# Optimization experiments

Measured on AMD Instinct MI355X. Metric: run time of the kernel, lower is better.

The kernel has to match this reference:

```python
import jax, jax.numpy as jnp
import numpy as np

KS = 7
DIM = 1024
HEADS = 16
B = 2048

def _rpb_index(ks):
    # Replicates the torch buffer: relative_position_index, shape [ks*ks, ks*ks]
    ch = np.arange(ks)
    coords = np.stack(np.meshgrid(ch, ch, indexing='ij')).reshape(2, -1)  # [2, N]
    rel = coords[:, :, None] - coords[:, None, :]                          # [2, N, N]
    rel = rel.transpose(1, 2, 0).copy()                                    # [N, N, 2]
    rel[:, :, 0] += ks - 1
    rel[:, :, 1] += ks - 1
    rel[:, :, 0] *= 2 * ks - 1
    idx = np.flipud(np.fliplr(rel.sum(-1)))
    return jnp.asarray(idx.copy())

def setup_inputs() -> dict:
    key = jax.random.key(0)
    ks = jax.random.split(key, 4)
    x = jax.random.normal(ks[0], (B, KS, KS, DIM), dtype=jnp.float32)
    qkv_w = jax.random.normal(ks[1], (3 * DIM, DIM), dtype=jnp.float32) * (DIM ** -0.5)
    qkv_b = jnp.zeros((3 * DIM,), dtype=jnp.float32)
    rpb = jax.random.normal(ks[2], (HEADS, 2 * KS - 1, 2 * KS - 1), dtype=jnp.float32) * 0.02
    proj_w = jax.random.normal(ks[3], (DIM, DIM), dtype=jnp.float32) * (DIM ** -0.5)
    proj_b = jnp.zeros((DIM,), dtype=jnp.float32)
    return {"x": x, "qkv_w": qkv_w, "qkv_b": qkv_b, "rpb": rpb, "proj_w": proj_w, "proj_b": proj_b}

def reference(x, qkv_w, qkv_b, rpb, proj_w, proj_b):
    Bn, H, W, C = x.shape
    ksz = H
    N = H * W
    heads = rpb.shape[0]
    hd = C // heads
    scale = hd ** -0.5
    idx = _rpb_index(ksz)  # [N, N] int

    qkv = x.reshape(Bn, N, C) @ qkv_w.T + qkv_b              # [B, N, 3C]
    qkv = qkv.reshape(Bn, N, 3, heads, hd).transpose(2, 0, 3, 1, 4)  # [3, B, h, N, hd]
    q, k, v = qkv[0] * scale, qkv[1], qkv[2]

    attn = jnp.einsum('bhnd,bhmd->bhnm', q, k)               # [B, h, N, N]
    # gather relative-position bias: rpb[h, 2k-1, 2k-1] -> flat [(2k-1)^2, h] -> [N, N, h]
    bias = rpb.transpose(1, 2, 0).reshape(-1, heads)[idx.reshape(-1)]
    bias = bias.reshape(N, N, heads).transpose(2, 0, 1)      # [h, N, N]
    attn = jax.nn.softmax(attn + bias[None], axis=-1)

    out = jnp.einsum('bhnm,bhmd->bhnd', attn, v)             # [B, h, N, hd]
    out = out.transpose(0, 2, 1, 3).reshape(Bn, H, W, C)
    return out @ proj_w.T + proj_b
```

## Files before the change

### kernel.cpp

```cpp
#include <hip/hip_runtime.h>


typedef _Float16 f16;
typedef _Float16 f16x8 __attribute__((ext_vector_type(8)));
typedef _Float16 f16x4 __attribute__((ext_vector_type(4)));
typedef float f32x4 __attribute__((ext_vector_type(4)));

#define G1P(p) ((const __attribute__((address_space(1))) unsigned int*)(p))
#define L3P(p) ((__attribute__((address_space(3))) unsigned int*)(p))

static const size_t MROW_MAX = 100351;

__global__ void cvt_kernel(const float* __restrict__ in, f16* __restrict__ out, int n4) {
  int i = blockIdx.x * blockDim.x + threadIdx.x;
  int stride = gridDim.x * blockDim.x;
  const float4* in4 = (const float4*)in;
  f16x4* out4 = (f16x4*)out;
  for (; i < n4; i += stride) {
    float4 v = in4[i];
    f16x4 o = { (f16)v.x, (f16)v.y, (f16)v.z, (f16)v.w };
    out4[i] = o;
  }
}

__global__ void bias_kernel(const float* __restrict__ rpb, float* __restrict__ bias_all) {
  int h = blockIdx.x;
  for (int e = threadIdx.x; e < 4096; e += blockDim.x) {
    int n = e >> 6, m = e & 63;
    float v = -1e30f;
    if (n < 49 && m < 49) {
      int in_ = n / 7, jn = n % 7, im = m / 7, jm = m % 7;
      v = rpb[h * 169 + (im - in_ + 6) * 13 + (jm - jn + 6)];
    }
    bias_all[h * 4096 + e] = v;
  }
}


#define VM4 asm volatile("s_waitcnt vmcnt(4)" ::: "memory")
#define VM0 asm volatile("s_waitcnt vmcnt(0)" ::: "memory")
#define NOVM ((void)0)
#define NOSTG ((void)0)

#define STAGE(GB, ROW0, COL0, LDSOFF)                                              \
  {                                                                                \
    const f16* s0_ = (GB) + (size_t)((ROW0) + wid * 32 + srow) * K + ((COL0) + sce); \
    __builtin_amdgcn_global_load_lds(G1P(s0_), L3P(lds + (LDSOFF) + wid * 2048), 16, 0, 0); \
    const f16* s1_ = s0_ + (size_t)16 * K;                                         \
    __builtin_amdgcn_global_load_lds(G1P(s1_), L3P(lds + (LDSOFF) + wid * 2048 + 1024), 16, 0, 0); \
  }

#define MFMA4(AREG, ROW)                                                           \
  acc[ROW][0] = __builtin_amdgcn_mfma_f32_16x16x32_f16(AREG, b0, acc[ROW][0], 0, 0, 0); \
  acc[ROW][1] = __builtin_amdgcn_mfma_f32_16x16x32_f16(AREG, b1, acc[ROW][1], 0, 0, 0); \
  acc[ROW][2] = __builtin_amdgcn_mfma_f32_16x16x32_f16(AREG, b2, acc[ROW][2], 0, 0, 0); \
  acc[ROW][3] = __builtin_amdgcn_mfma_f32_16x16x32_f16(AREG, b3, acc[ROW][3], 0, 0, 0);

#define PHASE(ABASE, BBASE, MH, STG, VMW)                                          \
  {                                                                                \
    f16x8 a0 = *(const f16x8*)((ABASE) + (wm * 128 + (MH) * 64 +  0 + l15) * 64 + swz); \
    f16x8 a1 = *(const f16x8*)((ABASE) + (wm * 128 + (MH) * 64 + 16 + l15) * 64 + swz); \
    f16x8 a2 = *(const f16x8*)((ABASE) + (wm * 128 + (MH) * 64 + 32 + l15) * 64 + swz); \
    f16x8 a3 = *(const f16x8*)((ABASE) + (wm * 128 + (MH) * 64 + 48 + l15) * 64 + swz); \
    if ((MH) == 0) {                                                               \
      b0 = *(const f16x8*)((BBASE) + (wn * 64 +  0 + l15) * 64 + swz);             \
      b1 = *(const f16x8*)((BBASE) + (wn * 64 + 16 + l15) * 64 + swz);             \
      b2 = *(const f16x8*)((BBASE) + (wn * 64 + 32 + l15) * 64 + swz);             \
      b3 = *(const f16x8*)((BBASE) + (wn * 64 + 48 + l15) * 64 + swz);             \
    }                                                                              \
    STG;                                                                           \
    __builtin_amdgcn_s_barrier();                                                  \
    asm volatile("s_waitcnt lgkmcnt(0)" ::: "memory");                             \
    __builtin_amdgcn_sched_barrier(0);                                             \
    __builtin_amdgcn_s_setprio(1);                                                 \
    MFMA4(a0, (MH) * 4 + 0) MFMA4(a1, (MH) * 4 + 1)                                \
    MFMA4(a2, (MH) * 4 + 2) MFMA4(a3, (MH) * 4 + 3)                                \
    __builtin_amdgcn_s_setprio(0);                                                 \
    VMW;                                                                           \
    __builtin_amdgcn_s_barrier();                                                  \
  }

template <typename OutT>
__global__ __launch_bounds__(512, 2)
void gemm256(const f16* __restrict__ A, const f16* __restrict__ B,
             const float* __restrict__ bias, OutT* __restrict__ C,
             int N, int K, int ntiles_n) {
  __shared__ char lds[131072];
  const int tid = threadIdx.x;
  const int wid = tid >> 6, ln = tid & 63;
  const int l15 = ln & 15, lhi = ln >> 4;
  const int wm = wid >> 2, wn = wid & 3;
  const int srow = ln >> 2;
  const int sce = (((ln & 3) ^ ((ln >> 3) & 3)) << 3);
  const int swz = ((lhi ^ ((l15 >> 1) & 3)) << 4);

  const int nblk = gridDim.x;
  const int wg = (blockIdx.x & 7) * (nblk >> 3) + (blockIdx.x >> 3);
  const int bn = wg % ntiles_n, bm = wg / ntiles_n;
  const int m0 = bm * 256, n0 = bn * 256;

  f32x4 acc[8][4];
#pragma unroll
  for (int i = 0; i < 8; ++i)
#pragma unroll
    for (int j = 0; j < 4; ++j) acc[i][j] = (f32x4){0.f, 0.f, 0.f, 0.f};
  f16x8 b0, b1, b2, b3;

  STAGE(A, m0, 0, 0);
  STAGE(B, n0, 0, 32768);
  STAGE(A, m0, 32, 16384);
  STAGE(B, n0, 32, 49152);
  STAGE(A, m0, 64, 65536);
  STAGE(B, n0, 64, 98304);
  VM4;
  __builtin_amdgcn_s_barrier();

  for (int i = 0; i < 7; ++i) {
    const int cT1k1 = (2 * i + 1) * 64 + 32;
    const int cT2k0 = (2 * i + 2) * 64;
    const int cT2k1 = cT2k0 + 32;
    const int cT3k0 = (2 * i + 3) * 64;
    PHASE(lds + 0,      lds + 32768,  0, STAGE(A, m0, cT1k1, 81920),  NOVM);
    PHASE(lds + 0,      lds + 32768,  1, STAGE(B, n0, cT1k1, 114688), NOVM);
    PHASE(lds + 16384,  lds + 49152,  0, STAGE(A, m0, cT2k0, 0),      NOVM);
    PHASE(lds + 16384,  lds + 49152,  1, STAGE(B, n0, cT2k0, 32768),  VM4);
    PHASE(lds + 65536,  lds + 98304,  0, STAGE(A, m0, cT2k1, 16384),  NOVM);
    PHASE(lds + 65536,  lds + 98304,  1, STAGE(B, n0, cT2k1, 49152),  NOVM);
    PHASE(lds + 81920,  lds + 114688, 0, STAGE(A, m0, cT3k0, 65536),  NOVM);
    PHASE(lds + 81920,  lds + 114688, 1, STAGE(B, n0, cT3k0, 98304),  VM4);
  }
  PHASE(lds + 0,      lds + 32768,  0, STAGE(A, m0, 15 * 64 + 32, 81920),  NOVM);
  PHASE(lds + 0,      lds + 32768,  1, STAGE(B, n0, 15 * 64 + 32, 114688), NOVM);
  PHASE(lds + 16384,  lds + 49152,  0, NOSTG, NOVM);
  PHASE(lds + 16384,  lds + 49152,  1, NOSTG, VM0);
  PHASE(lds + 65536,  lds + 98304,  0, NOSTG, NOVM);
  PHASE(lds + 65536,  lds + 98304,  1, NOSTG, NOVM);
  PHASE(lds + 81920,  lds + 114688, 0, NOSTG, NOVM);
  PHASE(lds + 81920,  lds + 114688, 1, NOSTG, NOVM);

  float bv[4];
#pragma unroll
  for (int j = 0; j < 4; ++j) bv[j] = bias[n0 + wn * 64 + j * 16 + l15];
#pragma unroll
  for (int ii = 0; ii < 8; ++ii)
#pragma unroll
    for (int j = 0; j < 4; ++j)
#pragma unroll
      for (int r = 0; r < 4; ++r) {
        int gr = m0 + wm * 128 + ii * 16 + lhi * 4 + r;
        int gc = n0 + wn * 64 + j * 16 + l15;
        C[(size_t)gr * N + gc] = (OutT)(acc[ii][j][r] + bv[j]);
      }
}

__global__ __launch_bounds__(64)
void attn_kernel(const f16* __restrict__ qkv,
                 const float* __restrict__ bias_all,
                 f16* __restrict__ out) {
  __shared__ char lds[16384];
  const int bh = blockIdx.x;
  const int b = bh >> 4, h = bh & 15;
  const int ln = threadIdx.x;
  const int l15 = ln & 15, lhi = ln >> 4;
  const size_t base = (size_t)b * 49;

  f16x8 qf[4][2];
#pragma unroll
  for (int t = 0; t < 4; ++t) {
    size_t row = base + t * 16 + l15;
    if (row > MROW_MAX) row = MROW_MAX;
    const f16* qp = qkv + row * 3072 + h * 64 + lhi * 8;
    qf[t][0] = *(const f16x8*)(qp);
    qf[t][1] = *(const f16x8*)(qp + 32);
  }
  {
    int rA = ln >> 3, lc = ln & 7;
#pragma unroll
    for (int c = 0; c < 8; ++c) {
      int r = c * 8 + rA;
      int ce = (lc ^ (r & 7)) << 3;
      size_t row = base + r;
      if (row > MROW_MAX) row = MROW_MAX;
      const f16* g = qkv + row * 3072 + 1024 + h * 64 + ce;
      __builtin_amdgcn_global_load_lds(G1P(g), L3P(lds + c * 1024), 16, 0, 0);
    }
  }
  {
    size_t row = base + ln;
    if (row > MROW_MAX) row = MROW_MAX;
    const f16* vp = qkv + row * 3072 + 2048 + h * 64;
    f16x8 vr[8];
#pragma unroll
    for (int j = 0; j < 8; ++j) vr[j] = *(const f16x8*)(vp + j * 8);
#pragma unroll
    for (int d = 0; d < 64; ++d)
      *(f16*)(lds + 8192 + d * 128 + ((ln * 2) ^ ((d & 7) << 4))) = vr[d >> 3][d & 7];
  }
  __syncthreads();

  f32x4 acc[4][4];
#pragma unroll
  for (int i = 0; i < 4; ++i)
#pragma unroll
    for (int j = 0; j < 4; ++j) acc[i][j] = (f32x4){0.f, 0.f, 0.f, 0.f};
#pragma unroll
  for (int kk = 0; kk < 2; ++kk) {
    f16x8 bf[4];
#pragma unroll
    for (int t = 0; t < 4; ++t) {
      int mr = t * 16 + l15;
      int pb = (kk * 64 + lhi * 16) ^ ((mr & 7) << 4);
      bf[t] = *(const f16x8*)(lds + mr * 128 + pb);
    }
#pragma unroll
    for (int i = 0; i < 4; ++i)
#pragma unroll
      for (int j = 0; j < 4; ++j)
        acc[i][j] = __builtin_amdgcn_mfma_f32_16x16x32_f16(qf[i][kk], bf[j], acc[i][j], 0, 0, 0);
  }

  const float* bb = bias_all + h * 4096;
#pragma unroll
  for (int i = 0; i < 4; ++i) {
#pragma unroll
    for (int r = 0; r < 4; ++r) {
      int n = i * 16 + lhi * 4 + r;
      float lv[4];
#pragma unroll
      for (int j = 0; j < 4; ++j)
        lv[j] = acc[i][j][r] * 0.125f + bb[n * 64 + j * 16 + l15];
      float Mx = fmaxf(fmaxf(lv[0], lv[1]), fmaxf(lv[2], lv[3]));
#pragma unroll
      for (int off = 1; off < 16; off <<= 1) Mx = fmaxf(Mx, __shfl_xor(Mx, off));
      float s = 0.f;
#pragma unroll
      for (int j = 0; j < 4; ++j) { lv[j] = __expf(lv[j] - Mx); s += lv[j]; }
#pragma unroll
      for (int off = 1; off < 16; off <<= 1) s += __shfl_xor(s, off);
      float inv = 1.f / s;
#pragma unroll
      for (int j = 0; j < 4; ++j) {
        int m = j * 16 + l15;
        *(f16*)(lds + n * 128 + ((m * 2) ^ ((n & 7) << 4))) = (f16)(lv[j] * inv);
      }
    }
  }
  __syncthreads();

  f32x4 o[4][4];
#pragma unroll
  for (int i = 0; i < 4; ++i)
#pragma unroll
    for (int j = 0; j < 4; ++j) o[i][j] = (f32x4){0.f, 0.f, 0.f, 0.f};
#pragma unroll
  for (int kk = 0; kk < 2; ++kk) {
    f16x8 af[4], bf[4];
#pragma unroll
    for (int t = 0; t < 4; ++t) {
      int nr = t * 16 + l15;
      int pb = (kk * 64 + lhi * 16) ^ ((nr & 7) << 4);
      af[t] = *(const f16x8*)(lds + nr * 128 + pb);
      bf[t] = *(const f16x8*)(lds + 8192 + nr * 128 + pb);
    }
#pragma unroll
    for (int i = 0; i < 4; ++i)
#pragma unroll
      for (int j = 0; j < 4; ++j)
        o[i][j] = __builtin_amdgcn_mfma_f32_16x16x32_f16(af[i], bf[j], o[i][j], 0, 0, 0);
  }
#pragma unroll
  for (int i = 0; i < 4; ++i)
#pragma unroll
    for (int j = 0; j < 4; ++j)
#pragma unroll
      for (int r = 0; r < 4; ++r) {
        int n = i * 16 + lhi * 4 + r;
        if (n < 49)
          out[(base + n) * 1024 + h * 64 + j * 16 + l15] = (f16)o[i][j][r];
      }
}

extern "C" void kernel_launch(void* const* d_in, const int* in_sizes, int n_in,
                              void* d_out, int out_size, void* d_ws, size_t ws_size,
                              hipStream_t stream) {
  const float* x      = (const float*)d_in[0];
  const float* qkv_w  = (const float*)d_in[1];
  const float* qkv_b  = (const float*)d_in[2];
  const float* rpb    = (const float*)d_in[3];
  const float* proj_w = (const float*)d_in[4];
  const float* proj_b = (const float*)d_in[5];
  float* out = (float*)d_out;

  char* ws = (char*)d_ws;
  f16*   x16      = (f16*)(ws);
  f16*   wq16     = (f16*)(ws + 205520896);
  f16*   wp16     = (f16*)(ws + 211812352);
  f16*   qkv16    = (f16*)(ws + 213909504);
  f16*   attn16   = (f16*)(ws + 830472192);
  float* bias_all = (float*)(ws + 1035993088);

  cvt_kernel<<<2048, 256, 0, stream>>>(x, x16, 102760448 / 4);
  cvt_kernel<<<1024, 256, 0, stream>>>(qkv_w, wq16, 3145728 / 4);
  cvt_kernel<<<512, 256, 0, stream>>>(proj_w, wp16, 1048576 / 4);
  bias_kernel<<<16, 64, 0, stream>>>(rpb, bias_all);

  gemm256<f16><<<4704, 512, 0, stream>>>(x16, wq16, qkv_b, qkv16, 3072, 1024, 12);
  attn_kernel<<<2048 * 16, 64, 0, stream>>>(qkv16, bias_all, attn16);
  gemm256<float><<<1568, 512, 0, stream>>>(attn16, wp16, proj_b, out, 1024, 1024, 4);
}
```

Measured before the change: 1.335 ms.

## Split attention block across two waves, read K from global, use exp2 softmax

The attention kernel now runs two waves per block, each owning 32 query rows and half of the V transpose staging. K fragments are read directly from global memory instead of being staged through LDS. The relative-position bias is stored transposed and pre-scaled by log2(e), so each lane fetches it with float4 loads and the softmax uses exp2f. This aims to cut per-wave serial work and the LDS staging of K, at the cost of both waves reading all of K from global or cache and needing an extra barrier.

```diff
diff --git a/kernel.cpp b/kernel.cpp
--- a/kernel.cpp
+++ b/kernel.cpp
@@ -23,19 +23,18 @@
   }
 }
 
-__global__ void bias_kernel(const float* __restrict__ rpb, float* __restrict__ bias_all) {
+__global__ void bias_kernel(const float* __restrict__ rpb, float* __restrict__ bias_t) {
   int h = blockIdx.x;
   for (int e = threadIdx.x; e < 4096; e += blockDim.x) {
-    int n = e >> 6, m = e & 63;
+    int m = e >> 6, n = e & 63;
     float v = -1e30f;
     if (n < 49 && m < 49) {
       int in_ = n / 7, jn = n % 7, im = m / 7, jm = m % 7;
       v = rpb[h * 169 + (im - in_ + 6) * 13 + (jm - jn + 6)];
     }
-    bias_all[h * 4096 + e] = v;
-  }
-}
-
+    bias_t[h * 4096 + e] = v * 1.44269504f;
+  }
+}
 
 #define VM4 asm volatile("s_waitcnt vmcnt(4)" ::: "memory")
 #define VM0 asm volatile("s_waitcnt vmcnt(0)" ::: "memory")
@@ -153,54 +152,47 @@
       }
 }
 
-__global__ __launch_bounds__(64)
+__global__ __launch_bounds__(128, 4)
 void attn_kernel(const f16* __restrict__ qkv,
-                 const float* __restrict__ bias_all,
+                 const float* __restrict__ bias_t,
                  f16* __restrict__ out) {
   __shared__ char lds[16384];
   const int bh = blockIdx.x;
   const int b = bh >> 4, h = bh & 15;
-  const int ln = threadIdx.x;
+  const int tid = threadIdx.x;
+  const int w = tid >> 6;
+  const int ln = tid & 63;
   const int l15 = ln & 15, lhi = ln >> 4;
   const size_t base = (size_t)b * 49;
-
-  f16x8 qf[4][2];
-#pragma unroll
-  for (int t = 0; t < 4; ++t) {
-    size_t row = base + t * 16 + l15;
+  const int nbase = w * 32;
+
+  f16x8 qf[2][2];
+#pragma unroll
+  for (int t = 0; t < 2; ++t) {
+    size_t row = base + nbase + t * 16 + l15;
     if (row > MROW_MAX) row = MROW_MAX;
     const f16* qp = qkv + row * 3072 + h * 64 + lhi * 8;
     qf[t][0] = *(const f16x8*)(qp);
     qf[t][1] = *(const f16x8*)(qp + 32);
   }
-  {
-    int rA = ln >> 3, lc = ln & 7;
-#pragma unroll
-    for (int c = 0; c < 8; ++c) {
-      int r = c * 8 + rA;
-      int ce = (lc ^ (r & 7)) << 3;
-      size_t row = base + r;
-      if (row > MROW_MAX) row = MROW_MAX;
-      const f16* g = qkv + row * 3072 + 1024 + h * 64 + ce;
-      __builtin_amdgcn_global_load_lds(G1P(g), L3P(lds + c * 1024), 16, 0, 0);
-    }
-  }
+
   {
     size_t row = base + ln;
     if (row > MROW_MAX) row = MROW_MAX;
-    const f16* vp = qkv + row * 3072 + 2048 + h * 64;
-    f16x8 vr[8];
-#pragma unroll
-    for (int j = 0; j < 8; ++j) vr[j] = *(const f16x8*)(vp + j * 8);
-#pragma unroll
-    for (int d = 0; d < 64; ++d)
-      *(f16*)(lds + 8192 + d * 128 + ((ln * 2) ^ ((d & 7) << 4))) = vr[d >> 3][d & 7];
-  }
-  __syncthreads();
-
-  f32x4 acc[4][4];
-#pragma unroll
-  for (int i = 0; i < 4; ++i)
+    const f16* vp = qkv + row * 3072 + 2048 + h * 64 + nbase;
+    f16x8 vr[4];
+#pragma unroll
+    for (int j = 0; j < 4; ++j) vr[j] = *(const f16x8*)(vp + j * 8);
+#pragma unroll
+    for (int dd = 0; dd < 32; ++dd) {
+      int d = nbase + dd;
+      *(f16*)(lds + 8192 + d * 128 + ((ln * 2) ^ ((d & 7) << 4))) = vr[dd >> 3][dd & 7];
+    }
+  }
+
+  f32x4 acc[2][4];
+#pragma unroll
+  for (int i = 0; i < 2; ++i)
 #pragma unroll
     for (int j = 0; j < 4; ++j) acc[i][j] = (f32x4){0.f, 0.f, 0.f, 0.f};
 #pragma unroll
@@ -208,33 +200,40 @@
     f16x8 bf[4];
 #pragma unroll
     for (int t = 0; t < 4; ++t) {
-      int mr = t * 16 + l15;
-      int pb = (kk * 64 + lhi * 16) ^ ((mr & 7) << 4);
-      bf[t] = *(const f16x8*)(lds + mr * 128 + pb);
-    }
-#pragma unroll
-    for (int i = 0; i < 4; ++i)
+      size_t row = base + t * 16 + l15;
+      if (row > MROW_MAX) row = MROW_MAX;
+      bf[t] = *(const f16x8*)(qkv + row * 3072 + 1024 + h * 64 + kk * 32 + lhi * 8);
+    }
+#pragma unroll
+    for (int i = 0; i < 2; ++i)
 #pragma unroll
       for (int j = 0; j < 4; ++j)
         acc[i][j] = __builtin_amdgcn_mfma_f32_16x16x32_f16(qf[i][kk], bf[j], acc[i][j], 0, 0, 0);
   }
 
-  const float* bb = bias_all + h * 4096;
-#pragma unroll
-  for (int i = 0; i < 4; ++i) {
+  __syncthreads();
+
+  const float SC = 0.125f * 1.44269504f;
+  const float* bb = bias_t + h * 4096;
+#pragma unroll
+  for (int i = 0; i < 2; ++i) {
+    float4 bq[4];
+#pragma unroll
+    for (int j = 0; j < 4; ++j)
+      bq[j] = *(const float4*)(bb + (j * 16 + l15) * 64 + nbase + i * 16 + lhi * 4);
 #pragma unroll
     for (int r = 0; r < 4; ++r) {
-      int n = i * 16 + lhi * 4 + r;
+      int n = nbase + i * 16 + lhi * 4 + r;
       float lv[4];
 #pragma unroll
       for (int j = 0; j < 4; ++j)
-        lv[j] = acc[i][j][r] * 0.125f + bb[n * 64 + j * 16 + l15];
+        lv[j] = acc[i][j][r] * SC + ((const float*)&bq[j])[r];
       float Mx = fmaxf(fmaxf(lv[0], lv[1]), fmaxf(lv[2], lv[3]));
 #pragma unroll
       for (int off = 1; off < 16; off <<= 1) Mx = fmaxf(Mx, __shfl_xor(Mx, off));
       float s = 0.f;
 #pragma unroll
-      for (int j = 0; j < 4; ++j) { lv[j] = __expf(lv[j] - Mx); s += lv[j]; }
+      for (int j = 0; j < 4; ++j) { lv[j] = exp2f(lv[j] - Mx); s += lv[j]; }
 #pragma unroll
       for (int off = 1; off < 16; off <<= 1) s += __shfl_xor(s, off);
       float inv = 1.f / s;
@@ -245,36 +244,38 @@
       }
     }
   }
-  __syncthreads();
-
-  f32x4 o[4][4];
-#pragma unroll
-  for (int i = 0; i < 4; ++i)
+
+  f32x4 o[2][4];
+#pragma unroll
+  for (int i = 0; i < 2; ++i)
 #pragma unroll
     for (int j = 0; j < 4; ++j) o[i][j] = (f32x4){0.f, 0.f, 0.f, 0.f};
 #pragma unroll
   for (int kk = 0; kk < 2; ++kk) {
-    f16x8 af[4], bf[4];
-#pragma unroll
-    for (int t = 0; t < 4; ++t) {
-      int nr = t * 16 + l15;
-      int pb = (kk * 64 + lhi * 16) ^ ((nr & 7) << 4);
-      af[t] = *(const f16x8*)(lds + nr * 128 + pb);
-      bf[t] = *(const f16x8*)(lds + 8192 + nr * 128 + pb);
-    }
-#pragma unroll
-    for (int i = 0; i < 4; ++i)
+    f16x8 af[2], bf[4];
+#pragma unroll
+    for (int t = 0; t < 2; ++t) {
+      int nr = nbase + t * 16 + l15;
+      af[t] = *(const f16x8*)(lds + nr * 128 + ((kk * 64 + lhi * 16) ^ ((nr & 7) << 4)));
+    }
+#pragma unroll
+    for (int u = 0; u < 4; ++u) {
+      int dr = u * 16 + l15;
+      bf[u] = *(const f16x8*)(lds + 8192 + dr * 128 + ((kk * 64 + lhi * 16) ^ ((dr & 7) << 4)));
+    }
+#pragma unroll
+    for (int i = 0; i < 2; ++i)
 #pragma unroll
       for (int j = 0; j < 4; ++j)
         o[i][j] = __builtin_amdgcn_mfma_f32_16x16x32_f16(af[i], bf[j], o[i][j], 0, 0, 0);
   }
 #pragma unroll
-  for (int i = 0; i < 4; ++i)
+  for (int i = 0; i < 2; ++i)
 #pragma unroll
     for (int j = 0; j < 4; ++j)
 #pragma unroll
       for (int r = 0; r < 4; ++r) {
-        int n = i * 16 + lhi * 4 + r;
+        int n = nbase + i * 16 + lhi * 4 + r;
         if (n < 49)
           out[(base + n) * 1024 + h * 64 + j * 16 + l15] = (f16)o[i][j][r];
       }
@@ -297,14 +298,14 @@
   f16*   wp16     = (f16*)(ws + 211812352);
   f16*   qkv16    = (f16*)(ws + 213909504);
   f16*   attn16   = (f16*)(ws + 830472192);
-  float* bias_all = (float*)(ws + 1035993088);
+  float* bias_t   = (float*)(ws + 1035993088);
 
   cvt_kernel<<<2048, 256, 0, stream>>>(x, x16, 102760448 / 4);
   cvt_kernel<<<1024, 256, 0, stream>>>(qkv_w, wq16, 3145728 / 4);
   cvt_kernel<<<512, 256, 0, stream>>>(proj_w, wp16, 1048576 / 4);
-  bias_kernel<<<16, 64, 0, stream>>>(rpb, bias_all);
+  bias_kernel<<<16, 64, 0, stream>>>(rpb, bias_t);
 
   gemm256<f16><<<4704, 512, 0, stream>>>(x16, wq16, qkv_b, qkv16, 3072, 1024, 12);
-  attn_kernel<<<2048 * 16, 64, 0, stream>>>(qkv16, bias_all, attn16);
+  attn_kernel<<<2048 * 16, 128, 0, stream>>>(qkv16, bias_t, attn16);
   gemm256<float><<<1568, 512, 0, stream>>>(attn16, wp16, proj_b, out, 1024, 1024, 4);
 }
```

New measurement: 1.384 ms. 1.04x slower.

## Prefetch f16 transposed bias into registers, use exp2 softmax, drop syncthreads in attention

Applied to the files above, without the earlier changes.

The bias table is now stored transposed as f16 with log2(e) folded in, and each lane loads it into registers up front instead of doing scattered fp32 loads during the softmax. V, Q and bias loads are issued together and the explicit barriers are swapped for a vmcnt wait, which is valid because the block is a single wave. Softmax uses exp2f with a combined scale, and setprio is placed around the MFMA bursts. The f16 bias uses -60000 as the mask value, which costs some precision but should still give a zero weight after exp2.

```diff
diff --git a/kernel.cpp b/kernel.cpp
--- a/kernel.cpp
+++ b/kernel.cpp
@@ -23,19 +23,18 @@
   }
 }
 
-__global__ void bias_kernel(const float* __restrict__ rpb, float* __restrict__ bias_all) {
+__global__ void bias_kernel(const float* __restrict__ rpb, f16* __restrict__ bias_t) {
   int h = blockIdx.x;
   for (int e = threadIdx.x; e < 4096; e += blockDim.x) {
-    int n = e >> 6, m = e & 63;
-    float v = -1e30f;
+    int m = e >> 6, n = e & 63;
+    float v = -60000.f;
     if (n < 49 && m < 49) {
       int in_ = n / 7, jn = n % 7, im = m / 7, jm = m % 7;
-      v = rpb[h * 169 + (im - in_ + 6) * 13 + (jm - jn + 6)];
-    }
-    bias_all[h * 4096 + e] = v;
-  }
-}
-
+      v = rpb[h * 169 + (im - in_ + 6) * 13 + (jm - jn + 6)] * 1.44269504f;
+    }
+    bias_t[h * 4096 + e] = (f16)v;
+  }
+}
 
 #define VM4 asm volatile("s_waitcnt vmcnt(4)" ::: "memory")
 #define VM0 asm volatile("s_waitcnt vmcnt(0)" ::: "memory")
@@ -155,7 +154,7 @@
 
 __global__ __launch_bounds__(64)
 void attn_kernel(const f16* __restrict__ qkv,
-                 const float* __restrict__ bias_all,
+                 const f16* __restrict__ bias_t,
                  f16* __restrict__ out) {
   __shared__ char lds[16384];
   const int bh = blockIdx.x;
@@ -164,15 +163,6 @@
   const int l15 = ln & 15, lhi = ln >> 4;
   const size_t base = (size_t)b * 49;
 
-  f16x8 qf[4][2];
-#pragma unroll
-  for (int t = 0; t < 4; ++t) {
-    size_t row = base + t * 16 + l15;
-    if (row > MROW_MAX) row = MROW_MAX;
-    const f16* qp = qkv + row * 3072 + h * 64 + lhi * 8;
-    qf[t][0] = *(const f16x8*)(qp);
-    qf[t][1] = *(const f16x8*)(qp + 32);
-  }
   {
     int rA = ln >> 3, lc = ln & 7;
 #pragma unroll
@@ -185,18 +175,38 @@
       __builtin_amdgcn_global_load_lds(G1P(g), L3P(lds + c * 1024), 16, 0, 0);
     }
   }
-  {
-    size_t row = base + ln;
+
+  size_t rowv = base + ln;
+  if (rowv > MROW_MAX) rowv = MROW_MAX;
+  const f16* vp = qkv + rowv * 3072 + 2048 + h * 64;
+  f16x8 vr[8];
+#pragma unroll
+  for (int j = 0; j < 8; ++j) vr[j] = *(const f16x8*)(vp + j * 8);
+
+  f16x8 qf[4][2];
+#pragma unroll
+  for (int t = 0; t < 4; ++t) {
+    size_t row = base + t * 16 + l15;
     if (row > MROW_MAX) row = MROW_MAX;
-    const f16* vp = qkv + row * 3072 + 2048 + h * 64;
-    f16x8 vr[8];
-#pragma unroll
-    for (int j = 0; j < 8; ++j) vr[j] = *(const f16x8*)(vp + j * 8);
-#pragma unroll
-    for (int d = 0; d < 64; ++d)
-      *(f16*)(lds + 8192 + d * 128 + ((ln * 2) ^ ((d & 7) << 4))) = vr[d >> 3][d & 7];
-  }
-  __syncthreads();
+    const f16* qp = qkv + row * 3072 + h * 64 + lhi * 8;
+    qf[t][0] = *(const f16x8*)(qp);
+    qf[t][1] = *(const f16x8*)(qp + 32);
+  }
+
+  const f16* bb = bias_t + h * 4096;
+  f16x4 bq[4][4];
+#pragma unroll
+  for (int i = 0; i < 4; ++i)
+#pragma unroll
+    for (int j = 0; j < 4; ++j)
+      bq[i][j] = *(const f16x4*)(bb + (j * 16 + l15) * 64 + i * 16 + lhi * 4);
+
+#pragma unroll
+  for (int d = 0; d < 64; ++d)
+    *(f16*)(lds + 8192 + d * 128 + ((ln * 2) ^ ((d & 7) << 4))) = vr[d >> 3][d & 7];
+
+  asm volatile("s_waitcnt vmcnt(0)" ::: "memory");
+  __builtin_amdgcn_sched_barrier(0);
 
   f32x4 acc[4][4];
 #pragma unroll
@@ -212,14 +222,16 @@
       int pb = (kk * 64 + lhi * 16) ^ ((mr & 7) << 4);
       bf[t] = *(const f16x8*)(lds + mr * 128 + pb);
     }
+    __builtin_amdgcn_s_setprio(1);
 #pragma unroll
     for (int i = 0; i < 4; ++i)
 #pragma unroll
       for (int j = 0; j < 4; ++j)
         acc[i][j] = __builtin_amdgcn_mfma_f32_16x16x32_f16(qf[i][kk], bf[j], acc[i][j], 0, 0, 0);
-  }
-
-  const float* bb = bias_all + h * 4096;
+    __builtin_amdgcn_s_setprio(0);
+  }
+
+  const float SC = 0.125f * 1.44269504f;
 #pragma unroll
   for (int i = 0; i < 4; ++i) {
 #pragma unroll
@@ -228,13 +240,13 @@
       float lv[4];
 #pragma unroll
       for (int j = 0; j < 4; ++j)
-        lv[j] = acc[i][j][r] * 0.125f + bb[n * 64 + j * 16 + l15];
+        lv[j] = acc[i][j][r] * SC + (float)bq[i][j][r];
       float Mx = fmaxf(fmaxf(lv[0], lv[1]), fmaxf(lv[2], lv[3]));
 #pragma unroll
       for (int off = 1; off < 16; off <<= 1) Mx = fmaxf(Mx, __shfl_xor(Mx, off));
       float s = 0.f;
 #pragma unroll
-      for (int j = 0; j < 4; ++j) { lv[j] = __expf(lv[j] - Mx); s += lv[j]; }
+      for (int j = 0; j < 4; ++j) { lv[j] = exp2f(lv[j] - Mx); s += lv[j]; }
 #pragma unroll
       for (int off = 1; off < 16; off <<= 1) s += __shfl_xor(s, off);
       float inv = 1.f / s;
@@ -245,7 +257,6 @@
       }
     }
   }
-  __syncthreads();
 
   f32x4 o[4][4];
 #pragma unroll
@@ -262,11 +273,13 @@
       af[t] = *(const f16x8*)(lds + nr * 128 + pb);
       bf[t] = *(const f16x8*)(lds + 8192 + nr * 128 + pb);
     }
+    __builtin_amdgcn_s_setprio(1);
 #pragma unroll
     for (int i = 0; i < 4; ++i)
 #pragma unroll
       for (int j = 0; j < 4; ++j)
         o[i][j] = __builtin_amdgcn_mfma_f32_16x16x32_f16(af[i], bf[j], o[i][j], 0, 0, 0);
+    __builtin_amdgcn_s_setprio(0);
   }
 #pragma unroll
   for (int i = 0; i < 4; ++i)
@@ -297,14 +310,14 @@
   f16*   wp16     = (f16*)(ws + 211812352);
   f16*   qkv16    = (f16*)(ws + 213909504);
   f16*   attn16   = (f16*)(ws + 830472192);
-  float* bias_all = (float*)(ws + 1035993088);
+  f16*   bias_t   = (f16*)(ws + 1035993088);
 
   cvt_kernel<<<2048, 256, 0, stream>>>(x, x16, 102760448 / 4);
   cvt_kernel<<<1024, 256, 0, stream>>>(qkv_w, wq16, 3145728 / 4);
   cvt_kernel<<<512, 256, 0, stream>>>(proj_w, wp16, 1048576 / 4);
-  bias_kernel<<<16, 64, 0, stream>>>(rpb, bias_all);
+  bias_kernel<<<16, 64, 0, stream>>>(rpb, bias_t);
 
   gemm256<f16><<<4704, 512, 0, stream>>>(x16, wq16, qkv_b, qkv16, 3072, 1024, 12);
-  attn_kernel<<<2048 * 16, 64, 0, stream>>>(qkv16, bias_all, attn16);
+  attn_kernel<<<2048 * 16, 64, 0, stream>>>(qkv16, bias_t, attn16);
   gemm256<float><<<1568, 512, 0, stream>>>(attn16, wp16, proj_b, out, 1024, 1024, 4);
 }
```

New measurement: 1.321 ms. Within noise of the previous version (-1.0%).
